# Performance work log

Hardware: AMD Instinct MI355X
Metric: run time of the kernel (lower is better)

Reference implementation:

```python
import jax, jax.numpy as jnp
import numpy as np

B, L, D, H = 2, 2048, 1024, 16
DH = D // H  # 64
LN_EPS = 1e-5


def setup_inputs() -> dict:
    key = jax.random.key(0)
    ks = jax.random.split(key, 16)
    s = 0.02
    return {
        "query": jax.random.normal(ks[0], (B, L, D), jnp.float32),
        "key": jax.random.normal(ks[1], (B, L, D), jnp.float32),
        "value": jax.random.normal(ks[2], (B, L, D), jnp.float32),
        "Wq": jax.random.normal(ks[3], (D, D), jnp.float32) * s,
        "bq": jnp.zeros((D,), jnp.float32),
        "Wk": jax.random.normal(ks[4], (D, D), jnp.float32) * s,
        "bk": jnp.zeros((D,), jnp.float32),
        "Wv": jax.random.normal(ks[5], (D, D), jnp.float32) * s,
        "bv": jnp.zeros((D,), jnp.float32),
        "Wo": jax.random.normal(ks[6], (D, D), jnp.float32) * s,
        "bo": jnp.zeros((D,), jnp.float32),
        "gamma": jnp.ones((D,), jnp.float32),
        "beta": jnp.zeros((D,), jnp.float32),
    }


def reference(query, key, value, Wq, bq, Wk, bk, Wv, bv, Wo, bo, gamma, beta):
    # Linear projections (torch Linear: x @ W.T + b)
    Q = jnp.einsum('bld,ed->ble', query, Wq) + bq
    K = jnp.einsum('bld,ed->ble', key, Wk) + bk
    V = jnp.einsum('bld,ed->ble', value, Wv) + bv
    # Faithful to the original: plain view/reshape WITHOUT head transpose.
    # [B, L, H*dh] -> [B*H, L, dh] (mixes sequence and head axes, as in source).
    Q = Q.reshape(B * H, L, DH)
    K = K.reshape(B * H, L, DH)
    V = V.reshape(B * H, L, DH)
    scale = DH ** (-0.5)
    scores = jnp.einsum('nqd,nkd->nqk', Q, K) * scale  # [B*H, L, L]
    attention = jax.nn.softmax(scores, axis=-1)
    context = jnp.einsum('nqk,nkd->nqd', attention, V)  # [B*H, L, dh]
    context = context.reshape(B, L, H * DH)
    out = jnp.einsum('bld,ed->ble', context, Wo) + bo
    out = out + query  # residual (dropout p=0.0 is identity)
    # LayerNorm over last dim
    mu = jnp.mean(out, axis=-1, keepdims=True)
    var = jnp.var(out, axis=-1, keepdims=True)
    out = (out - mu) * jax.lax.rsqrt(var + LN_EPS) * gamma + beta
    return (out, attention)
```

## Files before the change

kernel.cpp:

```cpp
#include <hip/hip_runtime.h>
#include <math.h>

#define SEQ   2048
#define DHD   64
#define NB    32
#define DMODEL 1024
#define MROWS 4096
#define ATTN_ELEMS 4194304
#define OUT0_ELEMS 4194304

typedef _Float16 h8 __attribute__((ext_vector_type(8)));
typedef _Float16 h4 __attribute__((ext_vector_type(4)));
typedef float    f4 __attribute__((ext_vector_type(4)));

#define MFMA16(a, b, c) __builtin_amdgcn_mfma_f32_16x16x32_f16((a), (b), (c), 0, 0, 0)

struct ConvArgs {
    const float* src[7];
    _Float16*    dst[7];
    int          n4[7];
};

__global__ __launch_bounds__(256) void k_convert(ConvArgs a) {
    const int t = blockIdx.x * 256 + threadIdx.x;
    const int j = blockIdx.y;
    if (t < a.n4[j]) {
        const float4 v = ((const float4*)a.src[j])[t];
        h4 h;
        h[0] = (_Float16)v.x; h[1] = (_Float16)v.y;
        h[2] = (_Float16)v.z; h[3] = (_Float16)v.w;
        ((h4*)a.dst[j])[t] = h;
    }
}

template <bool STORE_F16>
__device__ __forceinline__ void gemm_bt_body(
    const _Float16* __restrict__ A, const _Float16* __restrict__ Bt,
    const float* __restrict__ bias, _Float16* __restrict__ Ch,
    const float* __restrict__ resid, float* __restrict__ Cf,
    int Kd, int N)
{
    __shared__ __align__(16) _Float16 As[128 * 64];
    __shared__ __align__(16) _Float16 Bs[128 * 64];
    const int tid  = threadIdx.x;
    const int wave = tid >> 6, lane = tid & 63;
    const int lr = lane & 15, lk = lane >> 4;
    const int wm = (wave >> 1) * 64, wn = (wave & 1) * 64;
    const size_t rowA0 = (size_t)blockIdx.x * 128;
    const size_t rowB0 = (size_t)blockIdx.y * 128;

    f4 acc[4][4];
    const f4 fz = {0.f, 0.f, 0.f, 0.f};
#pragma unroll
    for (int i = 0; i < 4; i++)
#pragma unroll
        for (int j = 0; j < 4; j++) acc[i][j] = fz;

    for (int k0 = 0; k0 < Kd; k0 += 64) {
        __syncthreads();
#pragma unroll
        for (int i = 0; i < 4; i++) {
            const int idx = tid + i * 256;
            const int row = idx >> 3, c = idx & 7;
            *(uint4*)(&As[row * 64 + c * 8]) =
                *(const uint4*)(&A[(rowA0 + row) * (size_t)Kd + k0 + c * 8]);
            *(uint4*)(&Bs[row * 64 + c * 8]) =
                *(const uint4*)(&Bt[(rowB0 + row) * (size_t)Kd + k0 + c * 8]);
        }
        __syncthreads();
#pragma unroll
        for (int kk = 0; kk < 2; kk++) {
            h8 av[4], bv[4];
#pragma unroll
            for (int mt = 0; mt < 4; mt++)
                av[mt] = *(const h8*)(&As[(wm + mt * 16 + lr) * 64 + kk * 32 + lk * 8]);
#pragma unroll
            for (int nt = 0; nt < 4; nt++)
                bv[nt] = *(const h8*)(&Bs[(wn + nt * 16 + lr) * 64 + kk * 32 + lk * 8]);
#pragma unroll
            for (int mt = 0; mt < 4; mt++)
#pragma unroll
                for (int nt = 0; nt < 4; nt++)
                    acc[mt][nt] = MFMA16(av[mt], bv[nt], acc[mt][nt]);
        }
    }
#pragma unroll
    for (int mt = 0; mt < 4; mt++) {
#pragma unroll
        for (int nt = 0; nt < 4; nt++) {
#pragma unroll
            for (int r = 0; r < 4; r++) {
                const size_t row = rowA0 + wm + mt * 16 + lk * 4 + r;
                const int    col = (int)rowB0 + wn + nt * 16 + lr;
                const float  v   = acc[mt][nt][r] + bias[col];
                if constexpr (STORE_F16) {
                    Ch[row * (size_t)N + col] = (_Float16)v;
                } else {
                    Cf[row * (size_t)N + col] = v + resid[row * (size_t)N + col];
                }
            }
        }
    }
}

struct GemmPtrs {
    const _Float16* A[3];
    const _Float16* Bt[3];
    const float*    bias[3];
    _Float16*       C[3];
};

__global__ __launch_bounds__(256) void k_gemm_qkv(GemmPtrs p, int Kd, int N) {
    const int z = blockIdx.z;
    gemm_bt_body<true>(p.A[z], p.Bt[z], p.bias[z], p.C[z], nullptr, nullptr, Kd, N);
}

__global__ __launch_bounds__(256) void k_gemm_oproj(
    const _Float16* A, const _Float16* Bt, const float* bias,
    const float* resid, float* Cf, int Kd, int N) {
    gemm_bt_body<false>(A, Bt, bias, nullptr, resid, Cf, Kd, N);
}

__global__ __launch_bounds__(256) void k_transpose_v(
    const _Float16* __restrict__ Vh, _Float16* __restrict__ Vt) {
    __shared__ _Float16 T[64][72];
    const int n  = blockIdx.y;
    const int k0 = blockIdx.x * 64;
    const int tid = threadIdx.x;
    const _Float16* Vn = Vh + (size_t)n * (SEQ * DHD);
#pragma unroll
    for (int i = 0; i < 4; i++) {
        const int idx = tid + i * 256;
        const int kr = idx >> 4, c = idx & 15;
        *(h4*)(&T[kr][c * 4]) = *(const h4*)(&Vn[(size_t)(k0 + kr) * DHD + c * 4]);
    }
    __syncthreads();
    _Float16* Vtn = Vt + (size_t)n * (DHD * SEQ);
#pragma unroll
    for (int i = 0; i < 4; i++) {
        const int idx = tid + i * 256;
        const int d = idx >> 4, c = idx & 15;
        h4 h;
        h[0] = T[c * 4 + 0][d]; h[1] = T[c * 4 + 1][d];
        h[2] = T[c * 4 + 2][d]; h[3] = T[c * 4 + 3][d];
        *(h4*)(&Vtn[(size_t)d * SEQ + k0 + c * 4]) = h;
    }
}

__global__ __launch_bounds__(256) void k_attn_softmax(
    const _Float16* __restrict__ Qh, const _Float16* __restrict__ Kh,
    float* __restrict__ attn) {
    __shared__ __align__(16) _Float16 Ks[128 * 64];
    const int n  = blockIdx.y;
    const int q0 = blockIdx.x * 64;
    const int tid = threadIdx.x, wave = tid >> 6, lane = tid & 63;
    const int lr = lane & 15, lk = lane >> 4;
    const _Float16* Qn = Qh + (size_t)n * (SEQ * DHD);
    const _Float16* Kn = Kh + (size_t)n * (SEQ * DHD);

    h8 aq[2];
#pragma unroll
    for (int kk = 0; kk < 2; kk++)
        aq[kk] = *(const h8*)(&Qn[(size_t)(q0 + wave * 16 + lr) * DHD + kk * 32 + lk * 8]);

    float rs[4] = {0.f, 0.f, 0.f, 0.f};
    for (int kt = 0; kt < SEQ / 128; kt++) {
        __syncthreads();
#pragma unroll
        for (int i = 0; i < 4; i++) {
            const int idx = tid + i * 256;
            *(uint4*)(&Ks[idx * 8]) = *(const uint4*)(&Kn[(size_t)kt * (128 * DHD) + idx * 8]);
        }
        __syncthreads();
#pragma unroll
        for (int ct = 0; ct < 8; ct++) {
            f4 acc = {0.f, 0.f, 0.f, 0.f};
            const h8 b0 = *(const h8*)(&Ks[(ct * 16 + lr) * 64 + lk * 8]);
            const h8 b1 = *(const h8*)(&Ks[(ct * 16 + lr) * 64 + 32 + lk * 8]);
            acc = MFMA16(aq[0], b0, acc);
            acc = MFMA16(aq[1], b1, acc);
#pragma unroll
            for (int r = 0; r < 4; r++) rs[r] += __expf(acc[r] * 0.125f);
        }
    }
#pragma unroll
    for (int m = 1; m < 16; m <<= 1) {
#pragma unroll
        for (int r = 0; r < 4; r++) rs[r] += __shfl_xor(rs[r], m, 64);
    }
    float inv[4];
#pragma unroll
    for (int r = 0; r < 4; r++) inv[r] = 1.0f / rs[r];

    float* outn = attn + (size_t)n * ATTN_ELEMS;
    for (int kt = 0; kt < SEQ / 128; kt++) {
        __syncthreads();
#pragma unroll
        for (int i = 0; i < 4; i++) {
            const int idx = tid + i * 256;
            *(uint4*)(&Ks[idx * 8]) = *(const uint4*)(&Kn[(size_t)kt * (128 * DHD) + idx * 8]);
        }
        __syncthreads();
#pragma unroll
        for (int ct = 0; ct < 8; ct++) {
            f4 acc = {0.f, 0.f, 0.f, 0.f};
            const h8 b0 = *(const h8*)(&Ks[(ct * 16 + lr) * 64 + lk * 8]);
            const h8 b1 = *(const h8*)(&Ks[(ct * 16 + lr) * 64 + 32 + lk * 8]);
            acc = MFMA16(aq[0], b0, acc);
            acc = MFMA16(aq[1], b1, acc);
#pragma unroll
            for (int r = 0; r < 4; r++) {
                const float p = __expf(acc[r] * 0.125f) * inv[r];
                outn[(size_t)(q0 + wave * 16 + lk * 4 + r) * SEQ + kt * 128 + ct * 16 + lr] = p;
            }
        }
    }
}

__global__ __launch_bounds__(256) void k_context(
    const float* __restrict__ attn, const _Float16* __restrict__ Vt,
    _Float16* __restrict__ Ctx) {
    __shared__ __align__(16) _Float16 As[128 * 64];
    __shared__ __align__(16) _Float16 Bs[64 * 64];
    const int n  = blockIdx.y;
    const int q0 = blockIdx.x * 128;
    const int tid = threadIdx.x, wave = tid >> 6, lane = tid & 63;
    const int lr = lane & 15, lk = lane >> 4;
    const float* Pn = attn + (size_t)n * ATTN_ELEMS;
    const _Float16* Vn = Vt + (size_t)n * (DHD * SEQ);

    f4 acc[2][4];
    const f4 fz = {0.f, 0.f, 0.f, 0.f};
#pragma unroll
    for (int i = 0; i < 2; i++)
#pragma unroll
        for (int j = 0; j < 4; j++) acc[i][j] = fz;

    for (int k0 = 0; k0 < SEQ; k0 += 64) {
        __syncthreads();
#pragma unroll
        for (int i = 0; i < 8; i++) {
            const int idx = tid + i * 256;
            const int row = idx >> 4, c = idx & 15;
            const float4 v = *(const float4*)(&Pn[(size_t)(q0 + row) * SEQ + k0 + c * 4]);
            h4 h;
            h[0] = (_Float16)v.x; h[1] = (_Float16)v.y;
            h[2] = (_Float16)v.z; h[3] = (_Float16)v.w;
            *(h4*)(&As[row * 64 + c * 4]) = h;
        }
#pragma unroll
        for (int i = 0; i < 2; i++) {
            const int idx = tid + i * 256;
            const int row = idx >> 3, c = idx & 7;
            *(uint4*)(&Bs[row * 64 + c * 8]) =
                *(const uint4*)(&Vn[(size_t)row * SEQ + k0 + c * 8]);
        }
        __syncthreads();
#pragma unroll
        for (int kk = 0; kk < 2; kk++) {
            h8 av[2], bv[4];
#pragma unroll
            for (int mt = 0; mt < 2; mt++)
                av[mt] = *(const h8*)(&As[(wave * 32 + mt * 16 + lr) * 64 + kk * 32 + lk * 8]);
#pragma unroll
            for (int nt = 0; nt < 4; nt++)
                bv[nt] = *(const h8*)(&Bs[(nt * 16 + lr) * 64 + kk * 32 + lk * 8]);
#pragma unroll
            for (int mt = 0; mt < 2; mt++)
#pragma unroll
                for (int nt = 0; nt < 4; nt++)
                    acc[mt][nt] = MFMA16(av[mt], bv[nt], acc[mt][nt]);
        }
    }
#pragma unroll
    for (int mt = 0; mt < 2; mt++) {
#pragma unroll
        for (int nt = 0; nt < 4; nt++) {
#pragma unroll
            for (int r = 0; r < 4; r++) {
                const int q  = q0 + wave * 32 + mt * 16 + lk * 4 + r;
                const int dh = nt * 16 + lr;
                Ctx[(size_t)n * (SEQ * DHD) + (size_t)q * DHD + dh] = (_Float16)acc[mt][nt][r];
            }
        }
    }
}

__global__ __launch_bounds__(256) void k_layernorm(
    const float* __restrict__ X, const float* __restrict__ gamma,
    const float* __restrict__ beta, float* __restrict__ out) {
    __shared__ float red[8];
    const int row = blockIdx.x;
    const int tid = threadIdx.x;
    const float4 v = *(const float4*)(&X[(size_t)row * 1024 + tid * 4]);
    float s  = v.x + v.y + v.z + v.w;
    float ss = v.x * v.x + v.y * v.y + v.z * v.z + v.w * v.w;
#pragma unroll
    for (int m = 32; m >= 1; m >>= 1) {
        s  += __shfl_xor(s, m, 64);
        ss += __shfl_xor(ss, m, 64);
    }
    const int wave = tid >> 6, lane = tid & 63;
    if (lane == 0) { red[wave * 2] = s; red[wave * 2 + 1] = ss; }
    __syncthreads();
    s  = red[0] + red[2] + red[4] + red[6];
    ss = red[1] + red[3] + red[5] + red[7];
    const float mean = s * (1.0f / 1024.0f);
    const float var  = ss * (1.0f / 1024.0f) - mean * mean;
    const float rstd = 1.0f / sqrtf(var + 1e-5f);
    const float4 g = *(const float4*)(&gamma[tid * 4]);
    const float4 b = *(const float4*)(&beta[tid * 4]);
    float4 o;
    o.x = (v.x - mean) * rstd * g.x + b.x;
    o.y = (v.y - mean) * rstd * g.y + b.y;
    o.z = (v.z - mean) * rstd * g.z + b.z;
    o.w = (v.w - mean) * rstd * g.w + b.w;
    *(float4*)(&out[(size_t)row * 1024 + tid * 4]) = o;
}

extern "C" void kernel_launch(void* const* d_in, const int* in_sizes, int n_in,
                              void* d_out, int out_size, void* d_ws, size_t ws_size,
                              hipStream_t stream) {
    (void)in_sizes; (void)n_in; (void)out_size; (void)ws_size;
    const float* query = (const float*)d_in[0];
    const float* key   = (const float*)d_in[1];
    const float* value = (const float*)d_in[2];
    const float* Wq    = (const float*)d_in[3];
    const float* bq    = (const float*)d_in[4];
    const float* Wk    = (const float*)d_in[5];
    const float* bk    = (const float*)d_in[6];
    const float* Wv    = (const float*)d_in[7];
    const float* bv    = (const float*)d_in[8];
    const float* Wo    = (const float*)d_in[9];
    const float* bo    = (const float*)d_in[10];
    const float* gamma = (const float*)d_in[11];
    const float* beta  = (const float*)d_in[12];

    char* ws = (char*)d_ws;
    _Float16* XQ  = (_Float16*)(ws + 0);
    _Float16* XK  = (_Float16*)(ws + 8388608);
    _Float16* XV  = (_Float16*)(ws + 16777216);
    _Float16* WQh = (_Float16*)(ws + 25165824);
    _Float16* WKh = (_Float16*)(ws + 27262976);
    _Float16* WVh = (_Float16*)(ws + 29360128);
    _Float16* WOh = (_Float16*)(ws + 31457280);
    _Float16* QH  = (_Float16*)(ws + 33554432);
    _Float16* KH  = (_Float16*)(ws + 41943040);
    _Float16* VH  = (_Float16*)(ws + 50331648);
    _Float16* VT  = (_Float16*)(ws + 58720256);
    _Float16* CTX = (_Float16*)(ws + 67108864);
    float*    OPre = (float*)(ws + 0);

    float* outMain = (float*)d_out;
    float* attn    = outMain + OUT0_ELEMS;

    ConvArgs ca;
    ca.src[0] = query; ca.dst[0] = XQ;  ca.n4[0] = OUT0_ELEMS / 4;
    ca.src[1] = key;   ca.dst[1] = XK;  ca.n4[1] = OUT0_ELEMS / 4;
    ca.src[2] = value; ca.dst[2] = XV;  ca.n4[2] = OUT0_ELEMS / 4;
    ca.src[3] = Wq;    ca.dst[3] = WQh; ca.n4[3] = 1048576 / 4;
    ca.src[4] = Wk;    ca.dst[4] = WKh; ca.n4[4] = 1048576 / 4;
    ca.src[5] = Wv;    ca.dst[5] = WVh; ca.n4[5] = 1048576 / 4;
    ca.src[6] = Wo;    ca.dst[6] = WOh; ca.n4[6] = 1048576 / 4;
    k_convert<<<dim3(4096, 7), 256, 0, stream>>>(ca);

    GemmPtrs gp;
    gp.A[0] = XQ; gp.A[1] = XK; gp.A[2] = XV;
    gp.Bt[0] = WQh; gp.Bt[1] = WKh; gp.Bt[2] = WVh;
    gp.bias[0] = bq; gp.bias[1] = bk; gp.bias[2] = bv;
    gp.C[0] = QH; gp.C[1] = KH; gp.C[2] = VH;
    k_gemm_qkv<<<dim3(32, 8, 3), 256, 0, stream>>>(gp, DMODEL, DMODEL);

    k_transpose_v<<<dim3(32, 32), 256, 0, stream>>>(VH, VT);

    k_attn_softmax<<<dim3(32, 32), 256, 0, stream>>>(QH, KH, attn);

    k_context<<<dim3(16, 32), 256, 0, stream>>>(attn, VT, CTX);

    k_gemm_oproj<<<dim3(32, 8), 256, 0, stream>>>(CTX, WOh, bo, query, OPre, DMODEL, DMODEL);

    k_layernorm<<<4096, 256, 0, stream>>>(OPre, gamma, beta, outMain);
}
```

Measured before the change: 906.0 us.

## Fuse P@V context computation into the attention softmax kernel

The context kernel is folded into the second pass of the softmax kernel. Each probability tile is written to LDS in fp16 and multiplied with a V tile loaded alongside K, so the 512MB fp32 attention matrix no longer has to be read back from global memory. The attention stores also become nontemporal. In exchange the fused kernel uses more LDS and registers and does extra LDS traffic and MFMA work per block, which can lower occupancy.

```diff
diff --git a/kernel.cpp b/kernel.cpp
--- a/kernel.cpp
+++ b/kernel.cpp
@@ -147,16 +147,20 @@
     }
 }
 
-__global__ __launch_bounds__(256) void k_attn_softmax(
+__global__ __launch_bounds__(256) void k_attn_fused(
     const _Float16* __restrict__ Qh, const _Float16* __restrict__ Kh,
-    float* __restrict__ attn) {
+    const _Float16* __restrict__ Vt, float* __restrict__ attn,
+    _Float16* __restrict__ Ctx) {
     __shared__ __align__(16) _Float16 Ks[128 * 64];
+    __shared__ __align__(16) _Float16 Ps[64 * 136];
+    __shared__ __align__(16) _Float16 Vs[64 * 136];
     const int n  = blockIdx.y;
     const int q0 = blockIdx.x * 64;
     const int tid = threadIdx.x, wave = tid >> 6, lane = tid & 63;
     const int lr = lane & 15, lk = lane >> 4;
     const _Float16* Qn = Qh + (size_t)n * (SEQ * DHD);
     const _Float16* Kn = Kh + (size_t)n * (SEQ * DHD);
+    const _Float16* Vn = Vt + (size_t)n * (DHD * SEQ);
 
     h8 aq[2];
 #pragma unroll
@@ -192,6 +196,11 @@
 #pragma unroll
     for (int r = 0; r < 4; r++) inv[r] = 1.0f / rs[r];
 
+    f4 cacc[4];
+    const f4 fz = {0.f, 0.f, 0.f, 0.f};
+#pragma unroll
+    for (int nt = 0; nt < 4; nt++) cacc[nt] = fz;
+
     float* outn = attn + (size_t)n * ATTN_ELEMS;
     for (int kt = 0; kt < SEQ / 128; kt++) {
         __syncthreads();
@@ -199,6 +208,13 @@
         for (int i = 0; i < 4; i++) {
             const int idx = tid + i * 256;
             *(uint4*)(&Ks[idx * 8]) = *(const uint4*)(&Kn[(size_t)kt * (128 * DHD) + idx * 8]);
+        }
+#pragma unroll
+        for (int i = 0; i < 4; i++) {
+            const int idx = tid + i * 256;
+            const int d = idx >> 4, c = idx & 15;
+            *(uint4*)(&Vs[d * 136 + c * 8]) =
+                *(const uint4*)(&Vn[(size_t)d * SEQ + kt * 128 + c * 8]);
         }
         __syncthreads();
 #pragma unroll
@@ -211,77 +227,30 @@
 #pragma unroll
             for (int r = 0; r < 4; r++) {
                 const float p = __expf(acc[r] * 0.125f) * inv[r];
-                outn[(size_t)(q0 + wave * 16 + lk * 4 + r) * SEQ + kt * 128 + ct * 16 + lr] = p;
+                __builtin_nontemporal_store(p,
+                    &outn[(size_t)(q0 + wave * 16 + lk * 4 + r) * SEQ + kt * 128 + ct * 16 + lr]);
+                Ps[(wave * 16 + lk * 4 + r) * 136 + ct * 16 + lr] = (_Float16)p;
             }
         }
-    }
-}
-
-__global__ __launch_bounds__(256) void k_context(
-    const float* __restrict__ attn, const _Float16* __restrict__ Vt,
-    _Float16* __restrict__ Ctx) {
-    __shared__ __align__(16) _Float16 As[128 * 64];
-    __shared__ __align__(16) _Float16 Bs[64 * 64];
-    const int n  = blockIdx.y;
-    const int q0 = blockIdx.x * 128;
-    const int tid = threadIdx.x, wave = tid >> 6, lane = tid & 63;
-    const int lr = lane & 15, lk = lane >> 4;
-    const float* Pn = attn + (size_t)n * ATTN_ELEMS;
-    const _Float16* Vn = Vt + (size_t)n * (DHD * SEQ);
-
-    f4 acc[2][4];
-    const f4 fz = {0.f, 0.f, 0.f, 0.f};
-#pragma unroll
-    for (int i = 0; i < 2; i++)
-#pragma unroll
-        for (int j = 0; j < 4; j++) acc[i][j] = fz;
-
-    for (int k0 = 0; k0 < SEQ; k0 += 64) {
-        __syncthreads();
-#pragma unroll
-        for (int i = 0; i < 8; i++) {
-            const int idx = tid + i * 256;
-            const int row = idx >> 4, c = idx & 15;
-            const float4 v = *(const float4*)(&Pn[(size_t)(q0 + row) * SEQ + k0 + c * 4]);
-            h4 h;
-            h[0] = (_Float16)v.x; h[1] = (_Float16)v.y;
-            h[2] = (_Float16)v.z; h[3] = (_Float16)v.w;
-            *(h4*)(&As[row * 64 + c * 4]) = h;
-        }
-#pragma unroll
-        for (int i = 0; i < 2; i++) {
-            const int idx = tid + i * 256;
-            const int row = idx >> 3, c = idx & 7;
-            *(uint4*)(&Bs[row * 64 + c * 8]) =
-                *(const uint4*)(&Vn[(size_t)row * SEQ + k0 + c * 8]);
-        }
-        __syncthreads();
-#pragma unroll
-        for (int kk = 0; kk < 2; kk++) {
-            h8 av[2], bv[4];
-#pragma unroll
-            for (int mt = 0; mt < 2; mt++)
-                av[mt] = *(const h8*)(&As[(wave * 32 + mt * 16 + lr) * 64 + kk * 32 + lk * 8]);
+#pragma unroll
+        for (int kk2 = 0; kk2 < 4; kk2++) {
+            const h8 av = *(const h8*)(&Ps[(wave * 16 + lr) * 136 + kk2 * 32 + lk * 8]);
+            h8 bv[4];
 #pragma unroll
             for (int nt = 0; nt < 4; nt++)
-                bv[nt] = *(const h8*)(&Bs[(nt * 16 + lr) * 64 + kk * 32 + lk * 8]);
-#pragma unroll
-            for (int mt = 0; mt < 2; mt++)
-#pragma unroll
-                for (int nt = 0; nt < 4; nt++)
-                    acc[mt][nt] = MFMA16(av[mt], bv[nt], acc[mt][nt]);
-        }
-    }
-#pragma unroll
-    for (int mt = 0; mt < 2; mt++) {
-#pragma unroll
-        for (int nt = 0; nt < 4; nt++) {
-#pragma unroll
-            for (int r = 0; r < 4; r++) {
-                const int q  = q0 + wave * 32 + mt * 16 + lk * 4 + r;
-                const int dh = nt * 16 + lr;
-                Ctx[(size_t)n * (SEQ * DHD) + (size_t)q * DHD + dh] = (_Float16)acc[mt][nt][r];
-            }
+                bv[nt] = *(const h8*)(&Vs[(nt * 16 + lr) * 136 + kk2 * 32 + lk * 8]);
+#pragma unroll
+            for (int nt = 0; nt < 4; nt++)
+                cacc[nt] = MFMA16(av, bv[nt], cacc[nt]);
+        }
+    }
+#pragma unroll
+    for (int nt = 0; nt < 4; nt++) {
+#pragma unroll
+        for (int r = 0; r < 4; r++) {
+            const int q  = q0 + wave * 16 + lk * 4 + r;
+            const int dh = nt * 16 + lr;
+            Ctx[(size_t)n * (SEQ * DHD) + (size_t)q * DHD + dh] = (_Float16)cacc[nt][r];
         }
     }
 }
@@ -373,9 +342,7 @@
 
     k_transpose_v<<<dim3(32, 32), 256, 0, stream>>>(VH, VT);
 
-    k_attn_softmax<<<dim3(32, 32), 256, 0, stream>>>(QH, KH, attn);
-
-    k_context<<<dim3(16, 32), 256, 0, stream>>>(attn, VT, CTX);
+    k_attn_fused<<<dim3(32, 32), 256, 0, stream>>>(QH, KH, VT, attn, CTX);
 
     k_gemm_oproj<<<dim3(32, 8), 256, 0, stream>>>(CTX, WOh, bo, query, OPre, DMODEL, DMODEL);
 
```

New measurement: 834.5 us. 1.09x faster.
